# Kernel tuning notes

Measured on AMD Instinct MI355X. Metric: run time of the kernel, lower is better.

## Reference

```python
import jax, jax.numpy as jnp
import numpy as np

LP, LQ, B, D, H = 500, 64, 64, 256, 150  # lp, lq, batch_size, in_size, hidden_size*2


def setup_inputs() -> dict:
    key = jax.random.key(0)
    ks = jax.random.split(key, 12)
    s = 0.05
    f32 = jnp.float32
    return {
        "Up": jax.random.normal(ks[0], (LP, B, D), f32),
        "Uq": jax.random.normal(ks[1], (LQ, B, D), f32),
        "Wp": jax.random.normal(ks[2], (H, 2 * D), f32) * s,
        "Wq": jax.random.normal(ks[3], (H, 2 * D), f32) * s,
        "Wv": jax.random.normal(ks[4], (H, H), f32) * s,
        "Wg": jax.random.normal(ks[5], (4 * D, 4 * D), f32) * s,
        "V": jax.random.normal(ks[6], (B, H), f32),        # per-batch attention vector (squeezed [B,H,1])
        "v0": jax.random.normal(ks[7], (B, H), f32),       # initial GRU state self.v
        "W_ih": jax.random.normal(ks[8], (3 * H, 2 * D), f32) * s,
        "W_hh": jax.random.normal(ks[9], (3 * H, H), f32) * s,
        "b_ih": jax.random.normal(ks[10], (3 * H,), f32) * s,
        "b_hh": jax.random.normal(ks[11], (3 * H,), f32) * s,
    }


def reference(Up, Uq, Wp, Wq, Wv, Wg, V, v0, W_ih, W_hh, b_ih, b_hh):
    Din = Up.shape[2]
    # torch.cat([U, U[arange]], dim=2) == duplicate features
    Up2 = jnp.concatenate([Up, Up], axis=2)  # [lp, B, 2D]
    Uq2 = jnp.concatenate([Uq, Uq], axis=2)  # [lq, B, 2D]
    # Wq(Uq2) is loop-invariant in the original loop; hoist it (same math)
    Wuq = jnp.einsum('qbd,hd->qbh', Uq2, Wq)  # [lq, B, H]

    def gru_cell(x, h):
        gi = x @ W_ih.T + b_ih  # [B, 3H]
        gh = h @ W_hh.T + b_hh
        i_r, i_z, i_n = jnp.split(gi, 3, axis=1)
        h_r, h_z, h_n = jnp.split(gh, 3, axis=1)
        r = jax.nn.sigmoid(i_r + h_r)
        z = jax.nn.sigmoid(i_z + h_z)
        n = jnp.tanh(i_n + r * h_n)
        return (1.0 - z) * n + z * h

    def step(v, up_i):  # up_i: [B, 2D], v: [B, H]
        Wup = up_i @ Wp.T                                   # [B, H]
        x = jnp.tanh(Wup[None] + Wuq + (v @ Wv.T)[None])    # [lq, B, H]
        s = jnp.einsum('qbh,bh->bq', x, V)                  # bmm(x^T, V).squeeze
        a = jax.nn.softmax(s, axis=1)                       # [B, lq]
        c = jnp.einsum('bq,qbd->bd', a, Uq2)                # [B, 2D]
        r = jnp.concatenate([up_i, c], axis=1)              # [B, 4D]
        g = jax.nn.sigmoid(r @ Wg.T)
        r = g * r
        c_ = r[:, 2 * Din:]                                 # gated context -> GRU input
        v_new = gru_cell(c_, v)
        return v_new, v_new

    _, vs = jax.lax.scan(step, v0, Up2)  # [lp, B, H]
    # dropout is identity in eval mode
    return vs
```

## Files before the change

kernel.cpp:

```cpp
#include <hip/hip_runtime.h>
#include <hip/hip_fp16.h>

#define LP 500

typedef _Float16 h2f __attribute__((ext_vector_type(2)));
typedef _Float16 h8f __attribute__((ext_vector_type(8)));

constexpr size_t OFF_WVH2 = 0;
constexpr size_t OFF_WGF2 = 46208;
constexpr size_t OFF_WIH2 = 111744;
constexpr size_t OFF_WPF  = 227456;
constexpr size_t OFF_WQF  = 265856;
constexpr size_t OFF_WUQ  = 304256;
constexpr size_t OFF_P1   = 918656;
constexpr size_t OFF_WG1  = OFF_P1;
constexpr size_t OFF_GUH  = 5718656;
constexpr size_t OFF_UPT  = 13910656;
constexpr size_t OFF_UQT  = 22102656;
constexpr size_t OFF_UQT2 = OFF_UQT;
constexpr size_t WS_FLOATS = 23151232;

__device__ __forceinline__ float fast_rcp(float x) { return __builtin_amdgcn_rcpf(x); }
__device__ __forceinline__ float sigm(float x)   { return fast_rcp(1.f + __expf(-x)); }
__device__ __forceinline__ float tanh_f(float x) { return 1.f - 2.f * fast_rcp(1.f + __expf(2.f * x)); }

__global__ __launch_bounds__(256) void k_prep(const float* __restrict__ Wp, const float* __restrict__ Wq,
                                              const float* __restrict__ Wg, const float* __restrict__ Wv,
                                              const float* __restrict__ Whh, const float* __restrict__ Wih,
                                              float* __restrict__ ws) {
    int i = blockIdx.x * 256 + threadIdx.x;
    if (i < 46208) {
        int k2 = i / 608, m = i - k2 * 608;
        float lo = 0.f, hi = 0.f;
        if (k2 < 75 && m < 600) {
            if (m < 150) { lo = Wv[m * 150 + 2 * k2]; hi = Wv[m * 150 + 2 * k2 + 1]; }
            else { int mm = m - 150; lo = Whh[mm * 150 + 2 * k2]; hi = Whh[mm * 150 + 2 * k2 + 1]; }
        }
        ((h2f*)(ws + OFF_WVH2))[i] = h2f{(_Float16)lo, (_Float16)hi};
        return;
    }
    i -= 46208;
    if (i < 65536) {
        int k2 = i >> 9, j = i & 511;
        int d = 2 * k2;
        size_t r = (size_t)(512 + j) * 1024;
        float lo = Wg[r + 512 + d] + Wg[r + 768 + d];
        float hi = Wg[r + 512 + d + 1] + Wg[r + 768 + d + 1];
        ((h2f*)(ws + OFF_WGF2))[i] = h2f{(_Float16)lo, (_Float16)hi};
        return;
    }
    i -= 65536;
    if (i < 115712) {
        int k2 = i / 452, m = i - k2 * 452;
        float lo = 0.f, hi = 0.f;
        if (m < 450) { lo = Wih[m * 512 + 2 * k2]; hi = Wih[m * 512 + 2 * k2 + 1]; }
        ((h2f*)(ws + OFF_WIH2))[i] = h2f{(_Float16)lo, (_Float16)hi};
        return;
    }
    i -= 115712;
    if (i < 38400) { int h = i >> 8, d = i & 255; ws[OFF_WPF + i] = Wp[h * 512 + d] + Wp[h * 512 + 256 + d]; return; }
    i -= 38400;
    if (i < 38400) { int h = i >> 8, d = i & 255; ws[OFF_WQF + i] = Wq[h * 512 + d] + Wq[h * 512 + 256 + d]; return; }
    i -= 38400;
    if (i < 131072) { int j = i >> 8, d = i & 255; size_t r = (size_t)(512 + j) * 1024; ws[OFF_WG1 + i] = Wg[r + d] + Wg[r + 256 + d]; return; }
}

__global__ __launch_bounds__(256) void k_tr(const float* __restrict__ X, float* __restrict__ XT) {
    __shared__ float tile[64][65];
    size_t base = (size_t)blockIdx.x * 16384;
    for (int ph = 0; ph < 4; ++ph) {
        for (int i = threadIdx.x; i < 4096; i += 256) {
            int b = i >> 6, dl = i & 63;
            tile[b][dl] = X[base + (size_t)b * 256 + ph * 64 + dl];
        }
        __syncthreads();
        for (int i = threadIdx.x; i < 4096; i += 256) {
            int d = i >> 6, bl = i & 63;
            XT[base + (size_t)(ph * 64 + d) * 64 + bl] = tile[bl][d];
        }
        __syncthreads();
    }
}

__global__ __launch_bounds__(256) void k_gemm(const float* __restrict__ XT, const float* __restrict__ Wf,
                                              float* __restrict__ outF, _Float16* __restrict__ outH,
                                              int Hrows, int tilesPerT) {
    __shared__ float OL[64 * 33];
    int bidx = blockIdx.x;
    int t = bidx / tilesPerT, tile = bidx - t * tilesPerT;
    int w = threadIdx.x >> 6, lane = threadIdx.x & 63;
    int h0 = __builtin_amdgcn_readfirstlane(tile * 32 + w * 8);
    const float* x = XT + (size_t)t * 16384;
    float acc[8];
    const float* wr[8];
#pragma unroll
    for (int r = 0; r < 8; ++r) {
        int hr = h0 + r; if (hr >= Hrows) hr = Hrows - 1;
        wr[r] = Wf + (size_t)hr * 256;
        acc[r] = 0.f;
    }
    for (int d = 0; d < 256; d += 4) {
        float cv0 = x[(d + 0) * 64 + lane];
        float cv1 = x[(d + 1) * 64 + lane];
        float cv2 = x[(d + 2) * 64 + lane];
        float cv3 = x[(d + 3) * 64 + lane];
#pragma unroll
        for (int r = 0; r < 8; ++r) {
            float4 wv = *(const float4*)(wr[r] + d);
            acc[r] += cv0 * wv.x + cv1 * wv.y + cv2 * wv.z + cv3 * wv.w;
        }
    }
#pragma unroll
    for (int r = 0; r < 8; ++r) { int hl = w * 8 + r; OL[lane * 33 + hl] = acc[r]; }
    __syncthreads();
    int hbase = tile * 32;
    int nh = Hrows - hbase; if (nh > 32) nh = 32;
    for (int i = threadIdx.x; i < 64 * nh; i += 256) {
        int b = i / nh, hl = i - b * nh;
        float val = OL[b * 33 + hl];
        size_t idx = (size_t)t * 64 * Hrows + (size_t)b * Hrows + hbase + hl;
        if (outF) outF[idx] = val;
        else outH[idx] = (_Float16)val;
    }
}

__global__ __launch_bounds__(256) void k_uqt(const float* __restrict__ Uq, h2f* __restrict__ UqT2) {
    int b = blockIdx.x, d = threadIdx.x;
    for (int q2 = 0; q2 < 32; ++q2) {
        float lo = Uq[(size_t)(2 * q2) * 16384 + b * 256 + d];
        float hi = Uq[(size_t)(2 * q2 + 1) * 16384 + b * 256 + d];
        UqT2[(size_t)b * 8192 + q2 * 256 + d] = h2f{(_Float16)lo, (_Float16)hi};
    }
}

__global__ __launch_bounds__(768, 3) void k_scan10(
    const float* __restrict__ V, const float* __restrict__ v0,
    const float* __restrict__ bih, const float* __restrict__ bhh,
    const float* __restrict__ ws, float* __restrict__ out) {
    __shared__ __attribute__((aligned(16))) float red[3072];
    __shared__ __attribute__((aligned(16))) _Float16 vh[152];
    __shared__ float pbf[152];
    __shared__ float ghf[452];
    __shared__ float Vb[152];
    __shared__ float bihL[452];
    __shared__ float bhhL[452];
    __shared__ float vf[152];
    __shared__ float sa[64];
    __shared__ __attribute__((aligned(8))) h2f sah[32];
    __shared__ float ccf[256];
    __shared__ __attribute__((aligned(8))) h2f cchp[132];
    __shared__ __attribute__((aligned(8))) h2f c_p[256];
    __shared__ float gif[452];
    __shared__ __attribute__((aligned(16))) h2f uql[8192];
    __shared__ __attribute__((aligned(16))) h2f wihl[54 * 452];

    const int tid = threadIdx.x, b = blockIdx.x;
    const int lane = tid & 63;
    const h2f* Wvh2 = (const h2f*)(ws + OFF_WVH2);
    const h2f* Wih2 = (const h2f*)(ws + OFF_WIH2);
    const h2f* UqT2b = (const h2f*)(ws + OFF_UQT2) + (size_t)b * 8192;
    const float* WuqG = ws + OFF_WUQ;
    const float* P1 = ws + OFF_P1;
    const _Float16* GuH = (const _Float16*)(ws + OFF_GUH);

    const int p1_ks = tid / 152, p1_mq = tid - p1_ks * 152;
    const h2f* wv_base = Wvh2 + (size_t)(p1_ks * 15) * 608 + 4 * p1_mq;
    const int p2_qs = tid >> 6, p2_mq = tid & 63;
    const h2f* uq_base = uql + (size_t)(p2_qs * 4) * 256 + 4 * p2_mq;
    const int p3_ks = tid / 128, p3_mq = tid & 127;
    const int p4_ks = tid / 113, p4_mq = tid - p4_ks * 113;
    const h2f* wih_base = Wih2 + (size_t)(p4_ks * 44) * 452 + 4 * p4_mq;

    const h2f* Wgf2 = (const h2f*)(ws + OFF_WGF2);
    h8f wgr[22];
#pragma unroll
    for (int i = 0; i < 22; ++i) {
        int row = p3_ks * 22 + i;
        wgr[i] = (row < 128) ? *(const h8f*)(Wgf2 + (size_t)row * 512 + 4 * p3_mq) : h8f{};
    }

    const int w12 = tid >> 6;
    const int nq = (w12 < 4) ? 6 : 5;
    const int q0 = (w12 < 4) ? w12 * 6 : 24 + (w12 - 4) * 5;
    _Float16 wq[18];
#pragma unroll
    for (int i = 0; i < 6; ++i)
#pragma unroll
        for (int it = 0; it < 3; ++it) {
            int idx = lane + 64 * it;
            wq[i * 3 + it] = (_Float16)((i < nq && idx < 150) ? WuqG[(size_t)(q0 + i) * 9600 + b * 150 + idx] : 0.f);
        }

    {
        const h8f* s = (const h8f*)UqT2b;
        h8f* dstu = (h8f*)uql;
        for (int u = tid; u < 2048; u += 768) dstu[u] = s[u];
        h8f* dstw = (h8f*)wihl;
        for (int u = tid; u < 6102; u += 768) {
            int slot = u / 113, off = u - slot * 113;
            int ks = slot / 9, i = slot - ks * 9;
            dstw[u] = *(const h8f*)(Wih2 + (size_t)(ks * 44 + i) * 452 + off * 4);
        }
    }

    for (int i = tid; i < 150; i += 768) { Vb[i] = V[b * 150 + i]; float v = v0[b * 150 + i]; vf[i] = v; vh[i] = (_Float16)v; }
    for (int i = tid; i < 450; i += 768) { bihL[i] = bih[i]; bhhL[i] = bhh[i]; }
    if (tid < 2) vh[150 + tid] = (_Float16)0.f;
    if (tid < 4) cchp[128 + tid] = h2f{(_Float16)0.f, (_Float16)0.f};
    __syncthreads();

    for (int t = 0; t < LP; ++t) {
        float p1v = 0.f;
        if (tid < 150) p1v = P1[(size_t)t * 9600 + b * 150 + tid];
        float guv = 0.f;
        if (tid < 512) guv = (float)GuH[(size_t)t * 32768 + b * 512 + tid];

        if (tid < 760) {
            const h2f* vh2 = (const h2f*)vh;
            float a0 = 0.f, a1 = 0.f, a2 = 0.f, a3 = 0.f;
#pragma unroll 5
            for (int i = 0; i < 15; ++i) {
                h8f w = *(const h8f*)(wv_base + (size_t)i * 608);
                h2f x = vh2[p1_ks * 15 + i];
                a0 = __builtin_amdgcn_fdot2(h2f{w[0], w[1]}, x, a0, false);
                a1 = __builtin_amdgcn_fdot2(h2f{w[2], w[3]}, x, a1, false);
                a2 = __builtin_amdgcn_fdot2(h2f{w[4], w[5]}, x, a2, false);
                a3 = __builtin_amdgcn_fdot2(h2f{w[6], w[7]}, x, a3, false);
            }
            *(float4*)(red + p1_ks * 608 + 4 * p1_mq) = float4{a0, a1, a2, a3};
        }
        __syncthreads();
        if (tid < 600) {
            float s = red[tid] + red[608 + tid] + red[1216 + tid] + red[1824 + tid] + red[2432 + tid];
            if (tid < 150) pbf[tid] = s + p1v;
            else ghf[tid - 150] = s + bhhL[tid - 150];
        }
        __syncthreads();
        {
#pragma unroll
            for (int i = 0; i < 6; ++i) {
                if (i < nq) {
                    float part = 0.f;
#pragma unroll
                    for (int it = 0; it < 3; ++it) {
                        int idx = lane + 64 * it;
                        if (idx < 150)
                            part += tanh_f(pbf[idx] + (float)wq[i * 3 + it]) * Vb[idx];
                    }
                    part += __shfl_xor(part, 32); part += __shfl_xor(part, 16);
                    part += __shfl_xor(part, 8);  part += __shfl_xor(part, 4);
                    part += __shfl_xor(part, 2);  part += __shfl_xor(part, 1);
                    if (lane == 0) sa[q0 + i] = part;
                }
            }
        }
        __syncthreads();
        if (tid < 64) {
            float s = sa[tid];
            float m = s;
            m = fmaxf(m, __shfl_xor(m, 32)); m = fmaxf(m, __shfl_xor(m, 16));
            m = fmaxf(m, __shfl_xor(m, 8));  m = fmaxf(m, __shfl_xor(m, 4));
            m = fmaxf(m, __shfl_xor(m, 2));  m = fmaxf(m, __shfl_xor(m, 1));
            float e = __expf(s - m);
            float su = e;
            su += __shfl_xor(su, 32); su += __shfl_xor(su, 16); su += __shfl_xor(su, 8);
            su += __shfl_xor(su, 4);  su += __shfl_xor(su, 2);  su += __shfl_xor(su, 1);
            float a = e * fast_rcp(su);
            float an = __shfl_xor(a, 1);
            if ((tid & 1) == 0) sah[tid >> 1] = h2f{(_Float16)a, (_Float16)an};
        }
        __syncthreads();
        if (tid < 512) {
            float a0 = 0.f, a1 = 0.f, a2 = 0.f, a3 = 0.f;
#pragma unroll
            for (int i = 0; i < 4; ++i) {
                h8f u = *(const h8f*)(uq_base + (size_t)i * 256);
                h2f ap = sah[p2_qs * 4 + i];
                a0 = __builtin_amdgcn_fdot2(h2f{u[0], u[1]}, ap, a0, false);
                a1 = __builtin_amdgcn_fdot2(h2f{u[2], u[3]}, ap, a1, false);
                a2 = __builtin_amdgcn_fdot2(h2f{u[4], u[5]}, ap, a2, false);
                a3 = __builtin_amdgcn_fdot2(h2f{u[6], u[7]}, ap, a3, false);
            }
            *(float4*)(red + p2_qs * 256 + 4 * p2_mq) = float4{a0, a1, a2, a3};
        }
        __syncthreads();
        if (tid < 256) {
            float cc = 0.f;
#pragma unroll
            for (int s8 = 0; s8 < 8; ++s8) cc += red[s8 * 256 + tid];
            ccf[tid] = cc;
            float cn = __shfl_xor(cc, 1);
            if ((tid & 1) == 0) cchp[tid >> 1] = h2f{(_Float16)cc, (_Float16)cn};
        }
        __syncthreads();
        {
            float a0 = 0.f, a1 = 0.f, a2 = 0.f, a3 = 0.f;
#pragma unroll
            for (int i = 0; i < 22; ++i) {
                h2f cp = cchp[p3_ks * 22 + i];
                h8f w = wgr[i];
                a0 = __builtin_amdgcn_fdot2(h2f{w[0], w[1]}, cp, a0, false);
                a1 = __builtin_amdgcn_fdot2(h2f{w[2], w[3]}, cp, a1, false);
                a2 = __builtin_amdgcn_fdot2(h2f{w[4], w[5]}, cp, a2, false);
                a3 = __builtin_amdgcn_fdot2(h2f{w[6], w[7]}, cp, a3, false);
            }
            *(float4*)(red + p3_ks * 512 + 4 * p3_mq) = float4{a0, a1, a2, a3};
        }
        __syncthreads();
        if (tid < 512) {
            float s = guv;
#pragma unroll
            for (int s6 = 0; s6 < 6; ++s6) s += red[s6 * 512 + tid];
            float val = sigm(s) * ccf[tid & 255];
            float vn2 = __shfl_xor(val, 1);
            if ((tid & 1) == 0) c_p[tid >> 1] = h2f{(_Float16)val, (_Float16)vn2};
        }
        __syncthreads();
        if (tid < 678) {
            float a0 = 0.f, a1 = 0.f, a2 = 0.f, a3 = 0.f;
#pragma unroll
            for (int i = 0; i < 9; ++i) {
                h8f w = *(const h8f*)(wihl + (size_t)(p4_ks * 9 + i) * 452 + 4 * p4_mq);
                h2f cp = c_p[p4_ks * 44 + i];
                a0 = __builtin_amdgcn_fdot2(h2f{w[0], w[1]}, cp, a0, false);
                a1 = __builtin_amdgcn_fdot2(h2f{w[2], w[3]}, cp, a1, false);
                a2 = __builtin_amdgcn_fdot2(h2f{w[4], w[5]}, cp, a2, false);
                a3 = __builtin_amdgcn_fdot2(h2f{w[6], w[7]}, cp, a3, false);
            }
#pragma unroll 16
            for (int i = 9; i < 44; ++i) {
                int row = p4_ks * 44 + i;
                if (row < 256) {
                    h8f w = *(const h8f*)(wih_base + (size_t)i * 452);
                    h2f cp = c_p[row];
                    a0 = __builtin_amdgcn_fdot2(h2f{w[0], w[1]}, cp, a0, false);
                    a1 = __builtin_amdgcn_fdot2(h2f{w[2], w[3]}, cp, a1, false);
                    a2 = __builtin_amdgcn_fdot2(h2f{w[4], w[5]}, cp, a2, false);
                    a3 = __builtin_amdgcn_fdot2(h2f{w[6], w[7]}, cp, a3, false);
                }
            }
            *(float4*)(red + p4_ks * 456 + 4 * p4_mq) = float4{a0, a1, a2, a3};
        }
        __syncthreads();
        if (tid < 450) {
            gif[tid] = red[tid] + red[456 + tid] + red[912 + tid] + red[1368 + tid]
                     + red[1824 + tid] + red[2280 + tid];
        }
        __syncthreads();
        if (tid < 150) {
            float r = sigm(gif[tid] + bihL[tid] + ghf[tid]);
            float z = sigm(gif[150 + tid] + bihL[150 + tid] + ghf[150 + tid]);
            float n = tanh_f(gif[300 + tid] + bihL[300 + tid] + r * ghf[300 + tid]);
            float vn = (1.f - z) * n + z * vf[tid];
            vf[tid] = vn;
            vh[tid] = (_Float16)vn;
            out[(size_t)t * 9600 + b * 150 + tid] = vn;
        }
        __syncthreads();
    }
}

extern "C" void kernel_launch(void* const* d_in, const int* in_sizes, int n_in,
                              void* d_out, int out_size, void* d_ws, size_t ws_size,
                              hipStream_t stream) {
    const float* Up  = (const float*)d_in[0];
    const float* Uq  = (const float*)d_in[1];
    const float* Wp  = (const float*)d_in[2];
    const float* Wq  = (const float*)d_in[3];
    const float* Wv  = (const float*)d_in[4];
    const float* Wg  = (const float*)d_in[5];
    const float* V   = (const float*)d_in[6];
    const float* v0  = (const float*)d_in[7];
    const float* Wih = (const float*)d_in[8];
    const float* Whh = (const float*)d_in[9];
    const float* bih = (const float*)d_in[10];
    const float* bhh = (const float*)d_in[11];
    float* out = (float*)d_out;
    float* ws = (float*)d_ws;

    if (ws_size < WS_FLOATS * sizeof(float)) return;

    k_prep<<<1701, 256, 0, stream>>>(Wp, Wq, Wg, Wv, Whh, Wih, ws);
    k_tr<<<500, 256, 0, stream>>>(Up, ws + OFF_UPT);
    k_tr<<<64, 256, 0, stream>>>(Uq, ws + OFF_UQT);
    k_gemm<<<8000, 256, 0, stream>>>(ws + OFF_UPT, ws + OFF_WG1, nullptr, (_Float16*)(ws + OFF_GUH), 512, 16);
    k_gemm<<<2500, 256, 0, stream>>>(ws + OFF_UPT, ws + OFF_WPF, ws + OFF_P1, nullptr, 150, 5);
    k_gemm<<<320, 256, 0, stream>>>(ws + OFF_UQT, ws + OFF_WQF, ws + OFF_WUQ, nullptr, 150, 5);
    k_uqt<<<64, 256, 0, stream>>>(Uq, (h2f*)(ws + OFF_UQT2));
    k_scan10<<<64, 768, 0, stream>>>(V, v0, bih, bhh, ws, out);
}
```

Before: 6.419 ms.

## Precompute Uq·Wg per batch to fuse context and gate matvecs in scan

Adds a pre-kernel that computes M = Uq·Wg_ctx for each batch and query, so the per-step gate pre-activation can be formed directly from the attention weights (a·M) instead of first building the context and then multiplying by Wg. The context matvec and the gate matvec then run in parallel in one phase of the scan, which removes two barriers and a dependent stage from the serial 500-step loop. To free LDS for the 64x512 M tile, the shared W_ih tile is shrunk and some W_ih rows move into registers. This changes the rounding order, since M is stored in fp16, and it may add register pressure in the scan kernel.

```diff
diff --git a/kernel.cpp b/kernel.cpp
--- a/kernel.cpp
+++ b/kernel.cpp
@@ -16,6 +16,7 @@
 constexpr size_t OFF_WG1  = OFF_P1;
 constexpr size_t OFF_GUH  = 5718656;
 constexpr size_t OFF_UPT  = 13910656;
+constexpr size_t OFF_M2   = OFF_UPT;
 constexpr size_t OFF_UQT  = 22102656;
 constexpr size_t OFF_UQT2 = OFF_UQT;
 constexpr size_t WS_FLOATS = 23151232;
@@ -133,7 +134,38 @@
     }
 }
 
-__global__ __launch_bounds__(768, 3) void k_scan10(
+__global__ __launch_bounds__(512) void k_mgemm(const float* __restrict__ Uq,
+                                               const float* ws_ro,
+                                               h2f* M2) {
+    __shared__ _Float16 uqf[64 * 256];
+    int b = blockIdx.x, j = threadIdx.x;
+    const h2f* Wgf2 = (const h2f*)(ws_ro + OFF_WGF2);
+    for (int u = threadIdx.x; u < 16384; u += 512) {
+        int q = u >> 8, d = u & 255;
+        uqf[u] = (_Float16)Uq[(size_t)q * 16384 + b * 256 + d];
+    }
+    __syncthreads();
+    for (int qc = 0; qc < 8; ++qc) {
+        float acc[8];
+#pragma unroll
+        for (int i = 0; i < 8; ++i) acc[i] = 0.f;
+        for (int k2 = 0; k2 < 128; ++k2) {
+            h2f w = Wgf2[k2 * 512 + j];
+            float wlo = (float)w[0], whi = (float)w[1];
+#pragma unroll
+            for (int i = 0; i < 8; ++i) {
+                acc[i] += (float)uqf[(qc * 8 + i) * 256 + 2 * k2] * wlo
+                        + (float)uqf[(qc * 8 + i) * 256 + 2 * k2 + 1] * whi;
+            }
+        }
+#pragma unroll
+        for (int p = 0; p < 4; ++p)
+            M2[(size_t)b * 16384 + (size_t)(qc * 4 + p) * 512 + j] =
+                h2f{(_Float16)acc[2 * p], (_Float16)acc[2 * p + 1]};
+    }
+}
+
+__global__ __launch_bounds__(768, 3) void k_scan13(
     const float* __restrict__ V, const float* __restrict__ v0,
     const float* __restrict__ bih, const float* __restrict__ bhh,
     const float* __restrict__ ws, float* __restrict__ out) {
@@ -147,37 +179,26 @@
     __shared__ float vf[152];
     __shared__ float sa[64];
     __shared__ __attribute__((aligned(8))) h2f sah[32];
-    __shared__ float ccf[256];
-    __shared__ __attribute__((aligned(8))) h2f cchp[132];
     __shared__ __attribute__((aligned(8))) h2f c_p[256];
     __shared__ float gif[452];
     __shared__ __attribute__((aligned(16))) h2f uql[8192];
-    __shared__ __attribute__((aligned(16))) h2f wihl[54 * 452];
+    __shared__ __attribute__((aligned(16))) h2f m2l[16384];
+    __shared__ __attribute__((aligned(16))) h2f wihl[18 * 452];
 
     const int tid = threadIdx.x, b = blockIdx.x;
     const int lane = tid & 63;
     const h2f* Wvh2 = (const h2f*)(ws + OFF_WVH2);
     const h2f* Wih2 = (const h2f*)(ws + OFF_WIH2);
     const h2f* UqT2b = (const h2f*)(ws + OFF_UQT2) + (size_t)b * 8192;
+    const h2f* M2b = (const h2f*)(ws + OFF_M2) + (size_t)b * 16384;
     const float* WuqG = ws + OFF_WUQ;
     const float* P1 = ws + OFF_P1;
     const _Float16* GuH = (const _Float16*)(ws + OFF_GUH);
 
     const int p1_ks = tid / 152, p1_mq = tid - p1_ks * 152;
     const h2f* wv_base = Wvh2 + (size_t)(p1_ks * 15) * 608 + 4 * p1_mq;
-    const int p2_qs = tid >> 6, p2_mq = tid & 63;
-    const h2f* uq_base = uql + (size_t)(p2_qs * 4) * 256 + 4 * p2_mq;
-    const int p3_ks = tid / 128, p3_mq = tid & 127;
     const int p4_ks = tid / 113, p4_mq = tid - p4_ks * 113;
     const h2f* wih_base = Wih2 + (size_t)(p4_ks * 44) * 452 + 4 * p4_mq;
-
-    const h2f* Wgf2 = (const h2f*)(ws + OFF_WGF2);
-    h8f wgr[22];
-#pragma unroll
-    for (int i = 0; i < 22; ++i) {
-        int row = p3_ks * 22 + i;
-        wgr[i] = (row < 128) ? *(const h8f*)(Wgf2 + (size_t)row * 512 + 4 * p3_mq) : h8f{};
-    }
 
     const int w12 = tid >> 6;
     const int nq = (w12 < 4) ? 6 : 5;
@@ -191,22 +212,29 @@
             wq[i * 3 + it] = (_Float16)((i < nq && idx < 150) ? WuqG[(size_t)(q0 + i) * 9600 + b * 150 + idx] : 0.f);
         }
 
+    h8f wihr[12];
+#pragma unroll
+    for (int i = 0; i < 12; ++i)
+        wihr[i] = (tid < 678) ? *(const h8f*)(wih_base + (size_t)(3 + i) * 452) : h8f{};
+
     {
-        const h8f* s = (const h8f*)UqT2b;
-        h8f* dstu = (h8f*)uql;
-        for (int u = tid; u < 2048; u += 768) dstu[u] = s[u];
-        h8f* dstw = (h8f*)wihl;
-        for (int u = tid; u < 6102; u += 768) {
+        const h8f* su = (const h8f*)UqT2b;
+        h8f* du = (h8f*)uql;
+        for (int u = tid; u < 2048; u += 768) du[u] = su[u];
+        const h8f* sm = (const h8f*)M2b;
+        h8f* dm = (h8f*)m2l;
+        for (int u = tid; u < 4096; u += 768) dm[u] = sm[u];
+        h8f* dw = (h8f*)wihl;
+        for (int u = tid; u < 2034; u += 768) {
             int slot = u / 113, off = u - slot * 113;
-            int ks = slot / 9, i = slot - ks * 9;
-            dstw[u] = *(const h8f*)(Wih2 + (size_t)(ks * 44 + i) * 452 + off * 4);
+            int ks = slot / 3, i = slot - ks * 3;
+            dw[u] = *(const h8f*)(Wih2 + (size_t)(ks * 44 + i) * 452 + off * 4);
         }
     }
 
     for (int i = tid; i < 150; i += 768) { Vb[i] = V[b * 150 + i]; float v = v0[b * 150 + i]; vf[i] = v; vh[i] = (_Float16)v; }
     for (int i = tid; i < 450; i += 768) { bihL[i] = bih[i]; bhhL[i] = bhh[i]; }
     if (tid < 2) vh[150 + tid] = (_Float16)0.f;
-    if (tid < 4) cchp[128 + tid] = h2f{(_Float16)0.f, (_Float16)0.f};
     __syncthreads();
 
     for (int t = 0; t < LP; ++t) {
@@ -270,48 +298,41 @@
             if ((tid & 1) == 0) sah[tid >> 1] = h2f{(_Float16)a, (_Float16)an};
         }
         __syncthreads();
-        if (tid < 512) {
+        if (tid < 256) {
+            int cks = tid >> 6, cqd = tid & 63;
             float a0 = 0.f, a1 = 0.f, a2 = 0.f, a3 = 0.f;
 #pragma unroll
-            for (int i = 0; i < 4; ++i) {
-                h8f u = *(const h8f*)(uq_base + (size_t)i * 256);
-                h2f ap = sah[p2_qs * 4 + i];
+            for (int i = 0; i < 8; ++i) {
+                int q2 = cks * 8 + i;
+                h8f u = *(const h8f*)(uql + q2 * 256 + 4 * cqd);
+                h2f ap = sah[q2];
                 a0 = __builtin_amdgcn_fdot2(h2f{u[0], u[1]}, ap, a0, false);
                 a1 = __builtin_amdgcn_fdot2(h2f{u[2], u[3]}, ap, a1, false);
                 a2 = __builtin_amdgcn_fdot2(h2f{u[4], u[5]}, ap, a2, false);
                 a3 = __builtin_amdgcn_fdot2(h2f{u[6], u[7]}, ap, a3, false);
             }
-            *(float4*)(red + p2_qs * 256 + 4 * p2_mq) = float4{a0, a1, a2, a3};
-        }
-        __syncthreads();
-        if (tid < 256) {
-            float cc = 0.f;
-#pragma unroll
-            for (int s8 = 0; s8 < 8; ++s8) cc += red[s8 * 256 + tid];
-            ccf[tid] = cc;
-            float cn = __shfl_xor(cc, 1);
-            if ((tid & 1) == 0) cchp[tid >> 1] = h2f{(_Float16)cc, (_Float16)cn};
-        }
-        __syncthreads();
-        {
+            *(float4*)(red + cks * 256 + 4 * cqd) = float4{a0, a1, a2, a3};
+        } else {
+            int gt = tid - 256, gks = gt >> 7, gjq = gt & 127;
             float a0 = 0.f, a1 = 0.f, a2 = 0.f, a3 = 0.f;
 #pragma unroll
-            for (int i = 0; i < 22; ++i) {
-                h2f cp = cchp[p3_ks * 22 + i];
-                h8f w = wgr[i];
-                a0 = __builtin_amdgcn_fdot2(h2f{w[0], w[1]}, cp, a0, false);
-                a1 = __builtin_amdgcn_fdot2(h2f{w[2], w[3]}, cp, a1, false);
-                a2 = __builtin_amdgcn_fdot2(h2f{w[4], w[5]}, cp, a2, false);
-                a3 = __builtin_amdgcn_fdot2(h2f{w[6], w[7]}, cp, a3, false);
-            }
-            *(float4*)(red + p3_ks * 512 + 4 * p3_mq) = float4{a0, a1, a2, a3};
+            for (int i = 0; i < 8; ++i) {
+                int q2 = gks * 8 + i;
+                h8f m8 = *(const h8f*)(m2l + q2 * 512 + 4 * gjq);
+                h2f ap = sah[q2];
+                a0 = __builtin_amdgcn_fdot2(h2f{m8[0], m8[1]}, ap, a0, false);
+                a1 = __builtin_amdgcn_fdot2(h2f{m8[2], m8[3]}, ap, a1, false);
+                a2 = __builtin_amdgcn_fdot2(h2f{m8[4], m8[5]}, ap, a2, false);
+                a3 = __builtin_amdgcn_fdot2(h2f{m8[6], m8[7]}, ap, a3, false);
+            }
+            *(float4*)(red + 1024 + gks * 512 + 4 * gjq) = float4{a0, a1, a2, a3};
         }
         __syncthreads();
         if (tid < 512) {
-            float s = guv;
-#pragma unroll
-            for (int s6 = 0; s6 < 6; ++s6) s += red[s6 * 512 + tid];
-            float val = sigm(s) * ccf[tid & 255];
+            float g = guv + red[1024 + tid] + red[1536 + tid] + red[2048 + tid] + red[2560 + tid];
+            int dd = tid & 255;
+            float cc = red[dd] + red[256 + dd] + red[512 + dd] + red[768 + dd];
+            float val = sigm(g) * cc;
             float vn2 = __shfl_xor(val, 1);
             if ((tid & 1) == 0) c_p[tid >> 1] = h2f{(_Float16)val, (_Float16)vn2};
         }
@@ -319,16 +340,25 @@
         if (tid < 678) {
             float a0 = 0.f, a1 = 0.f, a2 = 0.f, a3 = 0.f;
 #pragma unroll
-            for (int i = 0; i < 9; ++i) {
-                h8f w = *(const h8f*)(wihl + (size_t)(p4_ks * 9 + i) * 452 + 4 * p4_mq);
+            for (int i = 0; i < 3; ++i) {
+                h8f w = *(const h8f*)(wihl + (size_t)(p4_ks * 3 + i) * 452 + 4 * p4_mq);
                 h2f cp = c_p[p4_ks * 44 + i];
                 a0 = __builtin_amdgcn_fdot2(h2f{w[0], w[1]}, cp, a0, false);
                 a1 = __builtin_amdgcn_fdot2(h2f{w[2], w[3]}, cp, a1, false);
                 a2 = __builtin_amdgcn_fdot2(h2f{w[4], w[5]}, cp, a2, false);
                 a3 = __builtin_amdgcn_fdot2(h2f{w[6], w[7]}, cp, a3, false);
             }
-#pragma unroll 16
-            for (int i = 9; i < 44; ++i) {
+#pragma unroll
+            for (int i = 3; i < 15; ++i) {
+                h8f w = wihr[i - 3];
+                h2f cp = c_p[p4_ks * 44 + i];
+                a0 = __builtin_amdgcn_fdot2(h2f{w[0], w[1]}, cp, a0, false);
+                a1 = __builtin_amdgcn_fdot2(h2f{w[2], w[3]}, cp, a1, false);
+                a2 = __builtin_amdgcn_fdot2(h2f{w[4], w[5]}, cp, a2, false);
+                a3 = __builtin_amdgcn_fdot2(h2f{w[6], w[7]}, cp, a3, false);
+            }
+#pragma unroll 15
+            for (int i = 15; i < 44; ++i) {
                 int row = p4_ks * 44 + i;
                 if (row < 256) {
                     h8f w = *(const h8f*)(wih_base + (size_t)i * 452);
@@ -387,5 +417,6 @@
     k_gemm<<<2500, 256, 0, stream>>>(ws + OFF_UPT, ws + OFF_WPF, ws + OFF_P1, nullptr, 150, 5);
     k_gemm<<<320, 256, 0, stream>>>(ws + OFF_UQT, ws + OFF_WQF, ws + OFF_WUQ, nullptr, 150, 5);
     k_uqt<<<64, 256, 0, stream>>>(Uq, (h2f*)(ws + OFF_UQT2));
-    k_scan10<<<64, 768, 0, stream>>>(V, v0, bih, bhh, ws, out);
-}
+    k_mgemm<<<64, 512, 0, stream>>>(Uq, ws, (h2f*)(ws + OFF_M2));
+    k_scan13<<<64, 768, 0, stream>>>(V, v0, bih, bhh, ws, out);
+}
```

After: 5.624 ms. -12.4%, faster.
